# Kernel tuning notes

Measured on AMD Instinct MI355X. Metric: run time of the kernel, lower is better.

Reference implementation:

```python
import jax, jax.numpy as jnp
import numpy as np

C_S, C_P, FEAT_DIM, NUM_BINS = 256, 128, 64, 22
MAX_DIST = 20.0
C_PAIR_PRE = 20
MAX_LEN = 2056.0


def get_index_embedding(indices, embed_size, max_len=MAX_LEN):
    # indices: (..., ) float; returns (..., embed_size) sinusoidal embedding
    K = jnp.arange(embed_size // 2, dtype=jnp.float32)
    ang = indices[..., None] * jnp.pi / (max_len ** (2.0 * K / embed_size))
    return jnp.concatenate([jnp.sin(ang), jnp.cos(ang)], axis=-1)


def rbf(D, D_min, D_max, D_count):
    # D: (...); returns (..., D_count) Gaussian RBF expansion
    D_mu = jnp.linspace(D_min, D_max, D_count)
    D_sigma = (D_max - D_min) / D_count
    return jnp.exp(-(((D[..., None] - D_mu) / D_sigma) ** 2))


def setup_inputs() -> dict:
    key = jax.random.key(0)
    ks = jax.random.split(key, 12)
    B, L = 1, 512
    total_edge = FEAT_DIM * 3 + NUM_BINS * 2 + C_PAIR_PRE  # 256
    inp = {
        "s": jax.random.normal(ks[0], (B, L, C_S), jnp.float32),
        "t": jax.random.normal(ks[1], (B, L, 3), jnp.float32),
        "sc_t": jax.random.normal(ks[2], (B, L, 3), jnp.float32),
        "pair_repr_pre": jax.random.normal(ks[3], (B, L, L, C_PAIR_PRE), jnp.float32),
        "p_mask": jnp.ones((B, L, L), jnp.float32),
        # linear_s_p: c_s -> feat_dim
        "W_sp": jax.random.normal(ks[4], (FEAT_DIM, C_S), jnp.float32) / np.sqrt(C_S),
        "b_sp": jnp.zeros((FEAT_DIM,), jnp.float32),
        # linear_relpos: feat_dim -> feat_dim
        "W_rp": jax.random.normal(ks[5], (FEAT_DIM, FEAT_DIM), jnp.float32) / np.sqrt(FEAT_DIM),
        "b_rp": jnp.zeros((FEAT_DIM,), jnp.float32),
        # edge_embedder: total_edge -> c_p -> c_p
        "W1": jax.random.normal(ks[6], (C_P, total_edge), jnp.float32) / np.sqrt(total_edge),
        "b1": jnp.zeros((C_P,), jnp.float32),
        "W2": jax.random.normal(ks[7], (C_P, C_P), jnp.float32) / np.sqrt(C_P),
        "b2": jnp.zeros((C_P,), jnp.float32),
    }
    return inp


def reference(s, t, sc_t, pair_repr_pre, p_mask, W_sp, b_sp, W_rp, b_rp, W1, b1, W2, b2):
    B, L, _ = s.shape
    # node projection then pairwise cross-concat -> (B, L, L, 2*feat_dim)
    p_i = jnp.einsum("bld,fd->blf", s, W_sp) + b_sp
    cross = jnp.concatenate([
        jnp.broadcast_to(p_i[:, :, None, :], (B, L, L, FEAT_DIM)),
        jnp.broadcast_to(p_i[:, None, :, :], (B, L, L, FEAT_DIM)),
    ], axis=-1)
    # relative-position sinusoidal embedding -> linear
    pos = jnp.arange(L, dtype=jnp.float32)[None, :]  # (1, L) broadcast over batch
    rel_pos = pos[:, :, None] - pos[:, None, :]      # (1, L, L)
    rel_pos = jnp.broadcast_to(rel_pos, (B, L, L))
    pos_emb = get_index_embedding(rel_pos, FEAT_DIM)
    relpos_feats = jnp.einsum("bijf,gf->bijg", pos_emb, W_rp) + b_rp
    # RBF distance expansions for backbone (t) and sidechain (sc_t) coords
    d_t = jnp.linalg.norm(t[:, :, None, :] - t[:, None, :, :], axis=-1)
    dist_feats = rbf(d_t, 0.0, MAX_DIST, NUM_BINS)
    d_sc = jnp.linalg.norm(sc_t[:, :, None, :] - sc_t[:, None, :, :], axis=-1)
    sc_feats = rbf(d_sc, 0.0, MAX_DIST, NUM_BINS)
    all_edge = jnp.concatenate([cross, relpos_feats, dist_feats, sc_feats, pair_repr_pre], axis=-1)
    # 2-layer MLP (dropout = 0 / eval mode)
    h = jax.nn.relu(jnp.einsum("bije,pe->bijp", all_edge, W1) + b1)
    edge_feats = jnp.einsum("bijp,qp->bijq", h, W2) + b2
    return edge_feats
```

## Files before the change

### kernel.cpp

```cpp
#include <hip/hip_runtime.h>
#include <hip/hip_bf16.h>


typedef __attribute__((ext_vector_type(8))) short v8s;
typedef __attribute__((ext_vector_type(4))) float v4f;

#define PI_F 3.14159265358979323846f

__global__ __launch_bounds__(256) void precompute_kernel(
    const float* __restrict__ s, const float* __restrict__ W_sp,
    const float* __restrict__ b_sp, const float* __restrict__ W_rp,
    const float* __restrict__ b_rp, const float* __restrict__ W1,
    const float* __restrict__ W2,
    __hip_bfloat16* __restrict__ p_bf, __hip_bfloat16* __restrict__ relT,
    __hip_bfloat16* __restrict__ W1b, __hip_bfloat16* __restrict__ W2b)
{
    const int b = blockIdx.x;
    const int tid = threadIdx.x;
    __shared__ float lds[128 * 65 + 8 * 256];

    if (b < 64) {
        float* Wt   = lds;
        float* srow = lds + 128 * 65;
        const int row0 = b * 8;
        const int f  = tid & 63;
        const int rh = tid >> 6;
        #pragma unroll
        for (int k = 0; k < 8; k++) {
            const int idx = tid + 256 * k;
            const int r = idx >> 8, d = idx & 255;
            srow[r * 256 + d] = s[(row0 + r) * 256 + d];
        }
        float acc0 = b_sp[f];
        float acc1 = acc0;
        for (int pass = 0; pass < 2; pass++) {
            __syncthreads();
            #pragma unroll
            for (int k = 0; k < 32; k++) {
                const int idx = tid + 256 * k;
                const int fs = idx >> 7, ds = idx & 127;
                Wt[ds * 65 + fs] = W_sp[fs * 256 + pass * 128 + ds];
            }
            __syncthreads();
            #pragma unroll 4
            for (int d = 0; d < 128; d++) {
                const float w = Wt[d * 65 + f];
                acc0 += srow[rh * 256 + pass * 128 + d] * w;
                acc1 += srow[(rh + 4) * 256 + pass * 128 + d] * w;
            }
        }
        p_bf[(row0 + rh) * 64 + f]     = __float2bfloat16(acc0);
        p_bf[(row0 + rh + 4) * 64 + f] = __float2bfloat16(acc1);
    } else if (b < 320) {
        float* WrT  = lds;
        float* femb = lds + 64 * 65;
        const int r0 = (b - 64) * 4;
        #pragma unroll
        for (int k = 0; k < 16; k++) {
            const int idx = tid + 256 * k;
            const int g = idx >> 6, ff = idx & 63;
            WrT[ff * 65 + g] = W_rp[g * 64 + ff];
        }
        {
            const int r = tid >> 6, c = tid & 63;
            const float rel = (float)(r0 + r - 511);
            const int K = c & 31;
            const float freq = powf(2056.0f, (2.0f * (float)K) / 64.0f);
            const float ang = rel * PI_F / freq;
            femb[r * 64 + c] = (c < 32) ? sinf(ang) : cosf(ang);
        }
        __syncthreads();
        const int g = tid & 63, r = tid >> 6;
        float acc = b_rp[g];
        #pragma unroll
        for (int ff = 0; ff < 64; ff++) acc += femb[r * 64 + ff] * WrT[ff * 65 + g];
        relT[(r0 + r) * 64 + g] = __float2bfloat16(acc);
    } else {
        #pragma unroll
        for (int k = 0; k < 2; k++) {
            const int idx4 = (b - 320) * 512 + k * 256 + tid;
            const int e = idx4 * 4;
            const float4 v = (e < 32768) ? *(const float4*)&W1[e]
                                         : *(const float4*)&W2[e - 32768];
            __hip_bfloat16* dst = (e < 32768) ? (W1b + e) : (W2b + (e - 32768));
            dst[0] = __float2bfloat16(v.x);
            dst[1] = __float2bfloat16(v.y);
            dst[2] = __float2bfloat16(v.z);
            dst[3] = __float2bfloat16(v.w);
        }
    }
}

__global__ __launch_bounds__(256, 4) void edge_main(
    const float* __restrict__ t3, const float* __restrict__ sc3,
    const float* __restrict__ pre,
    const float* __restrict__ b1, const float* __restrict__ b2,
    const __hip_bfloat16* __restrict__ p_bf, const __hip_bfloat16* __restrict__ relT,
    const __hip_bfloat16* __restrict__ W1b, const __hip_bfloat16* __restrict__ W2b,
    float* __restrict__ out)
{
    __shared__ char smem[64 * 264 * 2];
    __hip_bfloat16 (*Ash)[264] = (__hip_bfloat16(*)[264])smem;
    __hip_bfloat16 (*Hsh)[136] = (__hip_bfloat16(*)[136])smem;
    float          (*Cf)[132]  = (float(*)[132])smem;

    const int tid = threadIdx.x;
    const int blk = blockIdx.x;
    const int i  = blk >> 3;
    const int j0 = (blk & 7) << 6;

    const int wv   = tid >> 6;
    const int lane = tid & 63;
    const int l16  = lane & 15;
    const int quad = lane >> 4;
    const int nbase = wv * 32;

    const float b1v0 = b1[nbase + l16],      b1v1 = b1[nbase + 16 + l16];
    const float b2v0 = b2[nbase + l16],      b2v1 = b2[nbase + 16 + l16];
    const __hip_bfloat16* w1r0 = W1b + (nbase + l16) * 256 + quad * 8;
    const __hip_bfloat16* w1r1 = w1r0 + 16 * 256;
    const __hip_bfloat16* w2r0 = W2b + (nbase + l16) * 128 + quad * 8;
    const __hip_bfloat16* w2r1 = w2r0 + 16 * 128;
    const v8s p10 = *(const v8s*)w1r0;
    const v8s p11 = *(const v8s*)w1r1;
    const v8s p20 = *(const v8s*)w2r0;
    const v8s p21 = *(const v8s*)w2r1;

    #pragma unroll
    for (int c = tid; c < 512; c += 256) {
        const int r = c >> 3;
        const int cc = (c & 7) << 3;
        *(uint4*)&Ash[r][cc]       = *(const uint4*)&p_bf[i * 64 + cc];
        *(uint4*)&Ash[r][64 + cc]  = *(const uint4*)&p_bf[(j0 + r) * 64 + cc];
        *(uint4*)&Ash[r][128 + cc] = *(const uint4*)&relT[(i - (j0 + r) + 511) * 64 + cc];
    }
    for (int c = tid; c < 320; c += 256) {
        const int r = c / 5;
        const int f4 = (c % 5) * 4;
        const float4 v = *(const float4*)&pre[((size_t)i * 512 + j0 + r) * 20 + f4];
        Ash[r][236 + f4 + 0] = __float2bfloat16(v.x);
        Ash[r][236 + f4 + 1] = __float2bfloat16(v.y);
        Ash[r][236 + f4 + 2] = __float2bfloat16(v.z);
        Ash[r][236 + f4 + 3] = __float2bfloat16(v.w);
    }
    {
        const int r = tid >> 2;
        const int fo = (tid & 3) * 11;
        const int j = j0 + r;
        const float dxt = t3[i * 3 + 0] - t3[j * 3 + 0];
        const float dyt = t3[i * 3 + 1] - t3[j * 3 + 1];
        const float dzt = t3[i * 3 + 2] - t3[j * 3 + 2];
        const float dt = sqrtf(dxt * dxt + dyt * dyt + dzt * dzt);
        const float dxs = sc3[i * 3 + 0] - sc3[j * 3 + 0];
        const float dys = sc3[i * 3 + 1] - sc3[j * 3 + 1];
        const float dzs = sc3[i * 3 + 2] - sc3[j * 3 + 2];
        const float ds = sqrtf(dxs * dxs + dys * dys + dzs * dzs);
        #pragma unroll
        for (int q = 0; q < 11; q++) {
            const int f = fo + q;
            const float d = (f < 22) ? dt : ds;
            const int m = (f < 22) ? f : f - 22;
            const float x = (d - (float)m * (20.0f / 21.0f)) * 1.1f;
            Ash[r][192 + f] = __float2bfloat16(__expf(-x * x));
        }
    }
    __syncthreads();

    v4f acc[4][2];
    #pragma unroll
    for (int s4 = 0; s4 < 4; s4++)
        #pragma unroll
        for (int n = 0; n < 2; n++) acc[s4][n] = (v4f){0.f, 0.f, 0.f, 0.f};

    #pragma unroll
    for (int kt = 0; kt < 8; kt++) {
        const int ko = kt * 32 + quad * 8;
        const v8s a0 = *(const v8s*)&Ash[ 0 + l16][ko];
        const v8s a1 = *(const v8s*)&Ash[16 + l16][ko];
        const v8s a2 = *(const v8s*)&Ash[32 + l16][ko];
        const v8s a3 = *(const v8s*)&Ash[48 + l16][ko];
        const v8s bb0 = (kt == 0) ? p10 : *(const v8s*)(w1r0 + kt * 32);
        const v8s bb1 = (kt == 0) ? p11 : *(const v8s*)(w1r1 + kt * 32);
        acc[0][0] = __builtin_amdgcn_mfma_f32_16x16x32_bf16(a0, bb0, acc[0][0], 0, 0, 0);
        acc[1][0] = __builtin_amdgcn_mfma_f32_16x16x32_bf16(a1, bb0, acc[1][0], 0, 0, 0);
        acc[2][0] = __builtin_amdgcn_mfma_f32_16x16x32_bf16(a2, bb0, acc[2][0], 0, 0, 0);
        acc[3][0] = __builtin_amdgcn_mfma_f32_16x16x32_bf16(a3, bb0, acc[3][0], 0, 0, 0);
        acc[0][1] = __builtin_amdgcn_mfma_f32_16x16x32_bf16(a0, bb1, acc[0][1], 0, 0, 0);
        acc[1][1] = __builtin_amdgcn_mfma_f32_16x16x32_bf16(a1, bb1, acc[1][1], 0, 0, 0);
        acc[2][1] = __builtin_amdgcn_mfma_f32_16x16x32_bf16(a2, bb1, acc[2][1], 0, 0, 0);
        acc[3][1] = __builtin_amdgcn_mfma_f32_16x16x32_bf16(a3, bb1, acc[3][1], 0, 0, 0);
    }
    __syncthreads();

    #pragma unroll
    for (int s4 = 0; s4 < 4; s4++) {
        #pragma unroll
        for (int n = 0; n < 2; n++) {
            const float bv = n ? b1v1 : b1v0;
            #pragma unroll
            for (int r = 0; r < 4; r++) {
                float v = acc[s4][n][r] + bv;
                v = fmaxf(v, 0.0f);
                Hsh[s4 * 16 + quad * 4 + r][nbase + n * 16 + l16] = __float2bfloat16(v);
            }
        }
    }
    __syncthreads();

    v4f acc2[4][2];
    #pragma unroll
    for (int s4 = 0; s4 < 4; s4++)
        #pragma unroll
        for (int n = 0; n < 2; n++) acc2[s4][n] = (v4f){0.f, 0.f, 0.f, 0.f};

    #pragma unroll
    for (int kt = 0; kt < 4; kt++) {
        const int ko = kt * 32 + quad * 8;
        const v8s a0 = *(const v8s*)&Hsh[ 0 + l16][ko];
        const v8s a1 = *(const v8s*)&Hsh[16 + l16][ko];
        const v8s a2 = *(const v8s*)&Hsh[32 + l16][ko];
        const v8s a3 = *(const v8s*)&Hsh[48 + l16][ko];
        const v8s bb0 = (kt == 0) ? p20 : *(const v8s*)(w2r0 + kt * 32);
        const v8s bb1 = (kt == 0) ? p21 : *(const v8s*)(w2r1 + kt * 32);
        acc2[0][0] = __builtin_amdgcn_mfma_f32_16x16x32_bf16(a0, bb0, acc2[0][0], 0, 0, 0);
        acc2[1][0] = __builtin_amdgcn_mfma_f32_16x16x32_bf16(a1, bb0, acc2[1][0], 0, 0, 0);
        acc2[2][0] = __builtin_amdgcn_mfma_f32_16x16x32_bf16(a2, bb0, acc2[2][0], 0, 0, 0);
        acc2[3][0] = __builtin_amdgcn_mfma_f32_16x16x32_bf16(a3, bb0, acc2[3][0], 0, 0, 0);
        acc2[0][1] = __builtin_amdgcn_mfma_f32_16x16x32_bf16(a0, bb1, acc2[0][1], 0, 0, 0);
        acc2[1][1] = __builtin_amdgcn_mfma_f32_16x16x32_bf16(a1, bb1, acc2[1][1], 0, 0, 0);
        acc2[2][1] = __builtin_amdgcn_mfma_f32_16x16x32_bf16(a2, bb1, acc2[2][1], 0, 0, 0);
        acc2[3][1] = __builtin_amdgcn_mfma_f32_16x16x32_bf16(a3, bb1, acc2[3][1], 0, 0, 0);
    }
    __syncthreads();

    #pragma unroll
    for (int s4 = 0; s4 < 4; s4++) {
        #pragma unroll
        for (int n = 0; n < 2; n++) {
            const float bv = n ? b2v1 : b2v0;
            const int col = nbase + n * 16 + l16;
            #pragma unroll
            for (int r = 0; r < 4; r++) {
                Cf[s4 * 16 + quad * 4 + r][col] = acc2[s4][n][r] + bv;
            }
        }
    }
    __syncthreads();

    const size_t rowbase = (size_t)blk * 64;
    #pragma unroll
    for (int k = 0; k < 8; k++) {
        const int q = tid + k * 256;
        const int row = q >> 5;
        const int c4 = (q & 31) * 4;
        *(float4*)&out[(rowbase + row) * 128 + c4] = *(const float4*)&Cf[row][c4];
    }
}

extern "C" void kernel_launch(void* const* d_in, const int* in_sizes, int n_in,
                              void* d_out, int out_size, void* d_ws, size_t ws_size,
                              hipStream_t stream) {
    const float* s    = (const float*)d_in[0];
    const float* t3   = (const float*)d_in[1];
    const float* sc3  = (const float*)d_in[2];
    const float* pre  = (const float*)d_in[3];
    const float* W_sp = (const float*)d_in[5];
    const float* b_sp = (const float*)d_in[6];
    const float* W_rp = (const float*)d_in[7];
    const float* b_rp = (const float*)d_in[8];
    const float* W1   = (const float*)d_in[9];
    const float* b1   = (const float*)d_in[10];
    const float* W2   = (const float*)d_in[11];
    const float* b2   = (const float*)d_in[12];
    float* out = (float*)d_out;

    char* ws = (char*)d_ws;
    __hip_bfloat16* p_bf = (__hip_bfloat16*)(ws);
    __hip_bfloat16* relT = (__hip_bfloat16*)(ws + 65536);
    __hip_bfloat16* W1b  = (__hip_bfloat16*)(ws + 65536 + 131072);
    __hip_bfloat16* W2b  = (__hip_bfloat16*)(ws + 65536 + 131072 + 65536);

    precompute_kernel<<<344, 256, 0, stream>>>(s, W_sp, b_sp, W_rp, b_rp, W1, W2,
                                               p_bf, relT, W1b, W2b);
    edge_main<<<4096, 256, 0, stream>>>(t3, sc3, pre, b1, b2,
                                        p_bf, relT, W1b, W2b, out);
}
```

Measured before the change: 219.3 us.

## Swap MFMA operands, XOR-swizzle LDS, and store outputs directly from registers

The MFMA operands are swapped so weights form the A side and activations the B side. Each lane's accumulator then holds 4 consecutive output columns, which allows packed bf16 stores to LDS and direct float4 global stores without staging through shared memory. The LDS tiles use an unpadded layout with an XOR swizzle to avoid bank conflicts, which also shrinks shared memory and removes one barrier and one LDS round trip. Launch bounds are raised to 5 blocks per CU, trading register budget for occupancy. The direct output stores are 16-byte chunks strided across rows, so they may coalesce less well than before.

```diff
diff --git a/kernel.cpp b/kernel.cpp
--- a/kernel.cpp
+++ b/kernel.cpp
@@ -6,6 +6,11 @@
 typedef __attribute__((ext_vector_type(4))) float v4f;
 
 #define PI_F 3.14159265358979323846f
+
+__device__ __forceinline__ unsigned short f2bu(float x) {
+    __hip_bfloat16 h = __float2bfloat16(x);
+    return *reinterpret_cast<unsigned short*>(&h);
+}
 
 __global__ __launch_bounds__(256) void precompute_kernel(
     const float* __restrict__ s, const float* __restrict__ W_sp,
@@ -91,7 +96,7 @@
     }
 }
 
-__global__ __launch_bounds__(256, 4) void edge_main(
+__global__ __launch_bounds__(256, 5) void edge_main(
     const float* __restrict__ t3, const float* __restrict__ sc3,
     const float* __restrict__ pre,
     const float* __restrict__ b1, const float* __restrict__ b2,
@@ -99,10 +104,7 @@
     const __hip_bfloat16* __restrict__ W1b, const __hip_bfloat16* __restrict__ W2b,
     float* __restrict__ out)
 {
-    __shared__ char smem[64 * 264 * 2];
-    __hip_bfloat16 (*Ash)[264] = (__hip_bfloat16(*)[264])smem;
-    __hip_bfloat16 (*Hsh)[136] = (__hip_bfloat16(*)[136])smem;
-    float          (*Cf)[132]  = (float(*)[132])smem;
+    __shared__ char smem[32768];
 
     const int tid = threadIdx.x;
     const int blk = blockIdx.x;
@@ -113,38 +115,42 @@
     const int lane = tid & 63;
     const int l16  = lane & 15;
     const int quad = lane >> 4;
-    const int nbase = wv * 32;
-
-    const float b1v0 = b1[nbase + l16],      b1v1 = b1[nbase + 16 + l16];
-    const float b2v0 = b2[nbase + l16],      b2v1 = b2[nbase + 16 + l16];
-    const __hip_bfloat16* w1r0 = W1b + (nbase + l16) * 256 + quad * 8;
-    const __hip_bfloat16* w1r1 = w1r0 + 16 * 256;
-    const __hip_bfloat16* w2r0 = W2b + (nbase + l16) * 128 + quad * 8;
-    const __hip_bfloat16* w2r1 = w2r0 + 16 * 128;
-    const v8s p10 = *(const v8s*)w1r0;
-    const v8s p11 = *(const v8s*)w1r1;
-    const v8s p20 = *(const v8s*)w2r0;
-    const v8s p21 = *(const v8s*)w2r1;
+    const int cbase = wv * 32;
+
+    const float4 b1v0 = *(const float4*)&b1[cbase + quad * 4];
+    const float4 b1v1 = *(const float4*)&b1[cbase + 16 + quad * 4];
+    const float4 b2v0 = *(const float4*)&b2[cbase + quad * 4];
+    const float4 b2v1 = *(const float4*)&b2[cbase + 16 + quad * 4];
+    const __hip_bfloat16* w1m0 = W1b + (cbase + l16) * 256 + quad * 8;
+    const __hip_bfloat16* w1m1 = w1m0 + 16 * 256;
+    const __hip_bfloat16* w2m0 = W2b + (cbase + l16) * 128 + quad * 8;
+    const __hip_bfloat16* w2m1 = w2m0 + 16 * 128;
+    const v8s p10 = *(const v8s*)w1m0;
+    const v8s p11 = *(const v8s*)w1m1;
 
     #pragma unroll
     for (int c = tid; c < 512; c += 256) {
-        const int r = c >> 3;
-        const int cc = (c & 7) << 3;
-        *(uint4*)&Ash[r][cc]       = *(const uint4*)&p_bf[i * 64 + cc];
-        *(uint4*)&Ash[r][64 + cc]  = *(const uint4*)&p_bf[(j0 + r) * 64 + cc];
-        *(uint4*)&Ash[r][128 + cc] = *(const uint4*)&relT[(i - (j0 + r) + 511) * 64 + cc];
+        const int r  = c >> 3;
+        const int ck = c & 7;
+        const int px = (ck ^ (r & 7)) << 4;
+        char* rowp = smem + r * 512;
+        *(uint4*)(rowp + px)       = *(const uint4*)&p_bf[i * 64 + ck * 8];
+        *(uint4*)(rowp + 128 + px) = *(const uint4*)&p_bf[(j0 + r) * 64 + ck * 8];
+        *(uint4*)(rowp + 256 + px) = *(const uint4*)&relT[(i - (j0 + r) + 511) * 64 + ck * 8];
     }
     for (int c = tid; c < 320; c += 256) {
         const int r = c / 5;
-        const int f4 = (c % 5) * 4;
-        const float4 v = *(const float4*)&pre[((size_t)i * 512 + j0 + r) * 20 + f4];
-        Ash[r][236 + f4 + 0] = __float2bfloat16(v.x);
-        Ash[r][236 + f4 + 1] = __float2bfloat16(v.y);
-        Ash[r][236 + f4 + 2] = __float2bfloat16(v.z);
-        Ash[r][236 + f4 + 3] = __float2bfloat16(v.w);
+        const int q = c % 5;
+        const int col = 236 + q * 4;
+        const float4 v = *(const float4*)&pre[((size_t)i * 512 + j0 + r) * 20 + q * 4];
+        union { unsigned short s4[4]; uint2 u; } pk;
+        pk.s4[0] = f2bu(v.x); pk.s4[1] = f2bu(v.y);
+        pk.s4[2] = f2bu(v.z); pk.s4[3] = f2bu(v.w);
+        const int off = r * 512 + (((col >> 3) ^ (r & 7)) << 4) + ((col & 7) * 2);
+        *(uint2*)(smem + off) = pk.u;
     }
     {
-        const int r = tid >> 2;
+        const int r  = tid >> 2;
         const int fo = (tid & 3) * 11;
         const int j = j0 + r;
         const float dxt = t3[i * 3 + 0] - t3[j * 3 + 0];
@@ -155,105 +161,106 @@
         const float dys = sc3[i * 3 + 1] - sc3[j * 3 + 1];
         const float dzs = sc3[i * 3 + 2] - sc3[j * 3 + 2];
         const float ds = sqrtf(dxs * dxs + dys * dys + dzs * dzs);
+        char* rowp = smem + r * 512;
+        const int rx = r & 7;
         #pragma unroll
         for (int q = 0; q < 11; q++) {
             const int f = fo + q;
             const float d = (f < 22) ? dt : ds;
             const int m = (f < 22) ? f : f - 22;
             const float x = (d - (float)m * (20.0f / 21.0f)) * 1.1f;
-            Ash[r][192 + f] = __float2bfloat16(__expf(-x * x));
+            const int col = 192 + f;
+            const int off = (((col >> 3) ^ rx) << 4) + ((col & 7) * 2);
+            *(unsigned short*)(rowp + off) = f2bu(__expf(-x * x));
         }
     }
     __syncthreads();
 
-    v4f acc[4][2];
-    #pragma unroll
-    for (int s4 = 0; s4 < 4; s4++)
-        #pragma unroll
-        for (int n = 0; n < 2; n++) acc[s4][n] = (v4f){0.f, 0.f, 0.f, 0.f};
+    const int xorv = (l16 & 7) << 4;
+    v4f acc[2][4];
+    #pragma unroll
+    for (int mt = 0; mt < 2; mt++)
+        #pragma unroll
+        for (int nt = 0; nt < 4; nt++) acc[mt][nt] = (v4f){0.f, 0.f, 0.f, 0.f};
 
     #pragma unroll
     for (int kt = 0; kt < 8; kt++) {
-        const int ko = kt * 32 + quad * 8;
-        const v8s a0 = *(const v8s*)&Ash[ 0 + l16][ko];
-        const v8s a1 = *(const v8s*)&Ash[16 + l16][ko];
-        const v8s a2 = *(const v8s*)&Ash[32 + l16][ko];
-        const v8s a3 = *(const v8s*)&Ash[48 + l16][ko];
-        const v8s bb0 = (kt == 0) ? p10 : *(const v8s*)(w1r0 + kt * 32);
-        const v8s bb1 = (kt == 0) ? p11 : *(const v8s*)(w1r1 + kt * 32);
-        acc[0][0] = __builtin_amdgcn_mfma_f32_16x16x32_bf16(a0, bb0, acc[0][0], 0, 0, 0);
-        acc[1][0] = __builtin_amdgcn_mfma_f32_16x16x32_bf16(a1, bb0, acc[1][0], 0, 0, 0);
-        acc[2][0] = __builtin_amdgcn_mfma_f32_16x16x32_bf16(a2, bb0, acc[2][0], 0, 0, 0);
-        acc[3][0] = __builtin_amdgcn_mfma_f32_16x16x32_bf16(a3, bb0, acc[3][0], 0, 0, 0);
-        acc[0][1] = __builtin_amdgcn_mfma_f32_16x16x32_bf16(a0, bb1, acc[0][1], 0, 0, 0);
-        acc[1][1] = __builtin_amdgcn_mfma_f32_16x16x32_bf16(a1, bb1, acc[1][1], 0, 0, 0);
-        acc[2][1] = __builtin_amdgcn_mfma_f32_16x16x32_bf16(a2, bb1, acc[2][1], 0, 0, 0);
-        acc[3][1] = __builtin_amdgcn_mfma_f32_16x16x32_bf16(a3, bb1, acc[3][1], 0, 0, 0);
+        const int po = ((kt * 4 + quad) * 16) ^ xorv;
+        const v8s t0 = *(const v8s*)(smem + (l16     ) * 512 + po);
+        const v8s t1 = *(const v8s*)(smem + (l16 + 16) * 512 + po);
+        const v8s t2 = *(const v8s*)(smem + (l16 + 32) * 512 + po);
+        const v8s t3f = *(const v8s*)(smem + (l16 + 48) * 512 + po);
+        const v8s w0 = (kt == 0) ? p10 : *(const v8s*)(w1m0 + kt * 32);
+        const v8s w1f = (kt == 0) ? p11 : *(const v8s*)(w1m1 + kt * 32);
+        acc[0][0] = __builtin_amdgcn_mfma_f32_16x16x32_bf16(w0, t0,  acc[0][0], 0, 0, 0);
+        acc[0][1] = __builtin_amdgcn_mfma_f32_16x16x32_bf16(w0, t1,  acc[0][1], 0, 0, 0);
+        acc[0][2] = __builtin_amdgcn_mfma_f32_16x16x32_bf16(w0, t2,  acc[0][2], 0, 0, 0);
+        acc[0][3] = __builtin_amdgcn_mfma_f32_16x16x32_bf16(w0, t3f, acc[0][3], 0, 0, 0);
+        acc[1][0] = __builtin_amdgcn_mfma_f32_16x16x32_bf16(w1f, t0,  acc[1][0], 0, 0, 0);
+        acc[1][1] = __builtin_amdgcn_mfma_f32_16x16x32_bf16(w1f, t1,  acc[1][1], 0, 0, 0);
+        acc[1][2] = __builtin_amdgcn_mfma_f32_16x16x32_bf16(w1f, t2,  acc[1][2], 0, 0, 0);
+        acc[1][3] = __builtin_amdgcn_mfma_f32_16x16x32_bf16(w1f, t3f, acc[1][3], 0, 0, 0);
     }
     __syncthreads();
 
     #pragma unroll
-    for (int s4 = 0; s4 < 4; s4++) {
-        #pragma unroll
-        for (int n = 0; n < 2; n++) {
-            const float bv = n ? b1v1 : b1v0;
-            #pragma unroll
-            for (int r = 0; r < 4; r++) {
-                float v = acc[s4][n][r] + bv;
-                v = fmaxf(v, 0.0f);
-                Hsh[s4 * 16 + quad * 4 + r][nbase + n * 16 + l16] = __float2bfloat16(v);
-            }
+    for (int mt = 0; mt < 2; mt++) {
+        const float4 bv = mt ? b1v1 : b1v0;
+        const int col = cbase + mt * 16 + quad * 4;
+        #pragma unroll
+        for (int nt = 0; nt < 4; nt++) {
+            const int row = nt * 16 + l16;
+            union { unsigned short s4[4]; uint2 u; } pk;
+            pk.s4[0] = f2bu(fmaxf(acc[mt][nt][0] + bv.x, 0.f));
+            pk.s4[1] = f2bu(fmaxf(acc[mt][nt][1] + bv.y, 0.f));
+            pk.s4[2] = f2bu(fmaxf(acc[mt][nt][2] + bv.z, 0.f));
+            pk.s4[3] = f2bu(fmaxf(acc[mt][nt][3] + bv.w, 0.f));
+            const int off = row * 256 + (((col >> 3) ^ (row & 7)) << 4) + ((col & 7) * 2);
+            *(uint2*)(smem + off) = pk.u;
         }
     }
     __syncthreads();
 
-    v4f acc2[4][2];
-    #pragma unroll
-    for (int s4 = 0; s4 < 4; s4++)
-        #pragma unroll
-        for (int n = 0; n < 2; n++) acc2[s4][n] = (v4f){0.f, 0.f, 0.f, 0.f};
+    v4f acc2[2][4];
+    #pragma unroll
+    for (int mt = 0; mt < 2; mt++)
+        #pragma unroll
+        for (int nt = 0; nt < 4; nt++) acc2[mt][nt] = (v4f){0.f, 0.f, 0.f, 0.f};
 
     #pragma unroll
     for (int kt = 0; kt < 4; kt++) {
-        const int ko = kt * 32 + quad * 8;
-        const v8s a0 = *(const v8s*)&Hsh[ 0 + l16][ko];
-        const v8s a1 = *(const v8s*)&Hsh[16 + l16][ko];
-        const v8s a2 = *(const v8s*)&Hsh[32 + l16][ko];
-        const v8s a3 = *(const v8s*)&Hsh[48 + l16][ko];
-        const v8s bb0 = (kt == 0) ? p20 : *(const v8s*)(w2r0 + kt * 32);
-        const v8s bb1 = (kt == 0) ? p21 : *(const v8s*)(w2r1 + kt * 32);
-        acc2[0][0] = __builtin_amdgcn_mfma_f32_16x16x32_bf16(a0, bb0, acc2[0][0], 0, 0, 0);
-        acc2[1][0] = __builtin_amdgcn_mfma_f32_16x16x32_bf16(a1, bb0, acc2[1][0], 0, 0, 0);
-        acc2[2][0] = __builtin_amdgcn_mfma_f32_16x16x32_bf16(a2, bb0, acc2[2][0], 0, 0, 0);
-        acc2[3][0] = __builtin_amdgcn_mfma_f32_16x16x32_bf16(a3, bb0, acc2[3][0], 0, 0, 0);
-        acc2[0][1] = __builtin_amdgcn_mfma_f32_16x16x32_bf16(a0, bb1, acc2[0][1], 0, 0, 0);
-        acc2[1][1] = __builtin_amdgcn_mfma_f32_16x16x32_bf16(a1, bb1, acc2[1][1], 0, 0, 0);
-        acc2[2][1] = __builtin_amdgcn_mfma_f32_16x16x32_bf16(a2, bb1, acc2[2][1], 0, 0, 0);
-        acc2[3][1] = __builtin_amdgcn_mfma_f32_16x16x32_bf16(a3, bb1, acc2[3][1], 0, 0, 0);
-    }
-    __syncthreads();
-
-    #pragma unroll
-    for (int s4 = 0; s4 < 4; s4++) {
-        #pragma unroll
-        for (int n = 0; n < 2; n++) {
-            const float bv = n ? b2v1 : b2v0;
-            const int col = nbase + n * 16 + l16;
-            #pragma unroll
-            for (int r = 0; r < 4; r++) {
-                Cf[s4 * 16 + quad * 4 + r][col] = acc2[s4][n][r] + bv;
-            }
-        }
-    }
-    __syncthreads();
+        const int po = ((kt * 4 + quad) * 16) ^ xorv;
+        const v8s t0 = *(const v8s*)(smem + (l16     ) * 256 + po);
+        const v8s t1 = *(const v8s*)(smem + (l16 + 16) * 256 + po);
+        const v8s t2 = *(const v8s*)(smem + (l16 + 32) * 256 + po);
+        const v8s t3f = *(const v8s*)(smem + (l16 + 48) * 256 + po);
+        const v8s w0 = *(const v8s*)(w2m0 + kt * 32);
+        const v8s w1f = *(const v8s*)(w2m1 + kt * 32);
+        acc2[0][0] = __builtin_amdgcn_mfma_f32_16x16x32_bf16(w0, t0,  acc2[0][0], 0, 0, 0);
+        acc2[0][1] = __builtin_amdgcn_mfma_f32_16x16x32_bf16(w0, t1,  acc2[0][1], 0, 0, 0);
+        acc2[0][2] = __builtin_amdgcn_mfma_f32_16x16x32_bf16(w0, t2,  acc2[0][2], 0, 0, 0);
+        acc2[0][3] = __builtin_amdgcn_mfma_f32_16x16x32_bf16(w0, t3f, acc2[0][3], 0, 0, 0);
+        acc2[1][0] = __builtin_amdgcn_mfma_f32_16x16x32_bf16(w1f, t0,  acc2[1][0], 0, 0, 0);
+        acc2[1][1] = __builtin_amdgcn_mfma_f32_16x16x32_bf16(w1f, t1,  acc2[1][1], 0, 0, 0);
+        acc2[1][2] = __builtin_amdgcn_mfma_f32_16x16x32_bf16(w1f, t2,  acc2[1][2], 0, 0, 0);
+        acc2[1][3] = __builtin_amdgcn_mfma_f32_16x16x32_bf16(w1f, t3f, acc2[1][3], 0, 0, 0);
+    }
 
     const size_t rowbase = (size_t)blk * 64;
     #pragma unroll
-    for (int k = 0; k < 8; k++) {
-        const int q = tid + k * 256;
-        const int row = q >> 5;
-        const int c4 = (q & 31) * 4;
-        *(float4*)&out[(rowbase + row) * 128 + c4] = *(const float4*)&Cf[row][c4];
+    for (int mt = 0; mt < 2; mt++) {
+        const float4 bv = mt ? b2v1 : b2v0;
+        const int col = cbase + mt * 16 + quad * 4;
+        #pragma unroll
+        for (int nt = 0; nt < 4; nt++) {
+            const size_t row = rowbase + nt * 16 + l16;
+            float4 o;
+            o.x = acc2[mt][nt][0] + bv.x;
+            o.y = acc2[mt][nt][1] + bv.y;
+            o.z = acc2[mt][nt][2] + bv.z;
+            o.w = acc2[mt][nt][3] + bv.w;
+            *(float4*)&out[row * 128 + col] = o;
+        }
     }
 }
 
```

New measurement: 227.3 us. 1.04x slower.
